# Kernel optimization log

Measured on AMD Instinct MI355X. Metric: run time of the kernel, lower is better.

Reference implementation:

```python
import jax, jax.numpy as jnp
import numpy as np
from functools import reduce

N_QUBITS = 6
DIM = 2 ** N_QUBITS  # 64

# PauliZ expectation signs per wire: zsign[j, q] = +1 if bit q of basis state j is 0 else -1
# PennyLane convention: wire 0 is the most-significant bit.
_ZSIGN = jnp.asarray(1.0 - 2.0 * ((np.arange(DIM)[:, None] >> (N_QUBITS - 1 - np.arange(N_QUBITS))[None, :]) & 1), dtype=jnp.float32)  # [64, 6]

def _cnot_perm(c, t):
    # permutation p with new_state[j] = old_state[p[j]] for CNOT(control=c, target=t)
    idx = np.arange(DIM)
    cbit = (idx >> (N_QUBITS - 1 - c)) & 1
    return idx ^ (cbit << (N_QUBITS - 1 - t))

def _ring_perm(r):
    # compose the ring of CNOTs: CNOT(w, (w+r)%n) for w = 0..n-1 applied in order
    total = np.arange(DIM)
    for w in range(N_QUBITS):
        total = total[_cnot_perm(w, (w + r) % N_QUBITS)]
    return total

_RING = {r: jnp.asarray(_ring_perm(r)) for r in (1, 2)}

def _rot(phi, theta, omega):
    # PennyLane Rot(phi, theta, omega) = RZ(omega) @ RY(theta) @ RZ(phi)
    c = jnp.cos(theta / 2.0)
    s = jnp.sin(theta / 2.0)
    em = jnp.exp(-0.5j * (phi + omega))
    ep = jnp.exp(0.5j * (phi - omega))
    return jnp.stack([jnp.stack([em * c, -ep * s]),
                      jnp.stack([jnp.conj(ep) * s, jnp.conj(em) * c])])

def _strongly_entangling(psi, theta):
    # theta: [L, N_QUBITS, 3]; psi: [B, 64] complex
    L = theta.shape[0]
    for l in range(L):
        mats = [_rot(theta[l, w, 0], theta[l, w, 1], theta[l, w, 2]) for w in range(N_QUBITS)]
        U = reduce(jnp.kron, mats)  # [64, 64]; wire 0 = most significant, matches kron order
        psi = psi @ U.T
        r = l % (N_QUBITS - 1) + 1  # PennyLane default ranges
        psi = psi[:, _RING[r]]
    return psi

def setup_inputs() -> dict:
    key = jax.random.key(0)
    ks = jax.random.split(key, 12)
    B, D, H, NW = 131072, 64, 64, 5
    return {
        'x': jax.random.normal(ks[0], (B, D), dtype=jnp.float32),
        'W1': jax.random.normal(ks[1], (H, D), dtype=jnp.float32) * 0.1,
        'b1': jnp.zeros((H,), dtype=jnp.float32),
        'ln_g': jnp.ones((H,), dtype=jnp.float32),
        'ln_b': jnp.zeros((H,), dtype=jnp.float32),
        'W2': jax.random.normal(ks[2], (N_QUBITS, H), dtype=jnp.float32) * 0.1,
        'b2': jnp.zeros((N_QUBITS,), dtype=jnp.float32),
        'theta_shared': jax.random.normal(ks[3], (2, N_QUBITS, 3), dtype=jnp.float32) * 0.1,
        'theta_task': jax.random.normal(ks[4], (1, N_QUBITS, 3), dtype=jnp.float32) * 0.1,
        'Wc': jax.random.normal(ks[5], (NW, N_QUBITS), dtype=jnp.float32) * 0.1,
        'bc': jnp.zeros((NW,), dtype=jnp.float32),
    }

def reference(x, W1, b1, ln_g, ln_b, W2, b2, theta_shared, theta_task, Wc, bc):
    # --- encoder: Linear -> ReLU -> LayerNorm -> Linear -> Tanh ---
    h = jax.nn.relu(x @ W1.T + b1)
    mu = h.mean(-1, keepdims=True)
    var = ((h - mu) ** 2).mean(-1, keepdims=True)
    h = (h - mu) / jnp.sqrt(var + 1e-5) * ln_g + ln_b
    z = jnp.tanh(h @ W2.T + b2)  # [B, 6], in [-1, 1]
    # --- amplitude prep: RY(pi * z_q) on |0> per qubit -> product state ---
    half = (jnp.pi * z) / 2.0
    vec = jnp.stack([jnp.cos(half), jnp.sin(half)], axis=-1)  # [B, 6, 2]
    psi = vec[:, 0]
    for q in range(1, N_QUBITS):
        psi = (psi[:, :, None] * vec[:, q][:, None, :]).reshape(psi.shape[0], -1)
    psi = psi.astype(jnp.complex64)  # [B, 64]
    # --- VQC layers ---
    psi = _strongly_entangling(psi, theta_shared)
    psi = _strongly_entangling(psi, theta_task)
    # --- PauliZ expectation per wire ---
    probs = (psi * jnp.conj(psi)).real  # [B, 64]
    q_out = probs @ _ZSIGN  # [B, 6]
    # --- linear classifier ---
    return q_out @ Wc.T + bc
```

## Files before the change

### kernel.cpp

```cpp
#include <hip/hip_runtime.h>
#include <utility>

#define NQ 6
#define DIM 64

namespace {

constexpr int ring_entry(int r, int i) {
    int idx = i;
    for (int w = NQ - 1; w >= 0; --w) {
        int c = w;
        int t = (w + r) % NQ;
        int cbit = (idx >> (NQ - 1 - c)) & 1;
        idx ^= cbit << (NQ - 1 - t);
    }
    return idx;
}

constexpr int Mc(int L, int i) {
    if (L == 1) return ring_entry(1, i);
    if (L == 2) return ring_entry(1, ring_entry(2, i));
    if (L == 3) return ring_entry(1, ring_entry(2, ring_entry(1, i)));
    return i;
}

constexpr int Minv(int L, int p) {
    for (int i = 0; i < DIM; ++i) if (Mc(L, i) == p) return i;
    return -1;
}

}

__device__ __forceinline__ float swap1(float v) {
    return __int_as_float(__builtin_amdgcn_mov_dpp(__float_as_int(v), 0xB1, 0xF, 0xF, true));
}


template<int LY, int W, int d, int... Ls>
__device__ __forceinline__ void wire_inlane(float* sr, float* si,
        float A0r, float A0i, float B0r, float B0i,
        float A1r, float A1i, float B1r, float B1i,
        std::integer_sequence<int, Ls...>) {
    (([&] {
        if constexpr (Ls < (Ls ^ d)) {
            constexpr int la = Ls, lb = Ls ^ d;
            constexpr int ra = (Minv(LY, la) >> (5 - W)) & 1;
            constexpr int rb = (Minv(LY, lb) >> (5 - W)) & 1;
            const float cAar = ra ? A1r : A0r, cAai = ra ? A1i : A0i;
            const float cBar = ra ? B1r : B0r, cBai = ra ? B1i : B0i;
            const float cAbr = rb ? A1r : A0r, cAbi = rb ? A1i : A0i;
            const float cBbr = rb ? B1r : B0r, cBbi = rb ? B1i : B0i;
            const float mar = sr[la], mai = si[la];
            const float mbr = sr[lb], mbi = si[lb];
            sr[la] = cAar*mar - cAai*mai + cBar*mbr - cBai*mbi;
            si[la] = cAar*mai + cAai*mar + cBar*mbi + cBai*mbr;
            sr[lb] = cAbr*mbr - cAbi*mbi + cBbr*mar - cBbi*mai;
            si[lb] = cAbr*mbi + cAbi*mbr + cBbr*mai + cBbi*mar;
        }
    }()), ...);
}

template<int LY, int W, int... Ls>
__device__ __forceinline__ void wire_cross0(float* sr, float* si,
        float A0r, float A0i, float B0r, float B0i,
        float A1r, float A1i, float B1r, float B1i,
        std::integer_sequence<int, Ls...>) {
    (([&] {
        constexpr int r = (Minv(LY, Ls) >> (5 - W)) & 1;
        const float cAr = r ? A1r : A0r, cAi = r ? A1i : A0i;
        const float cBr = r ? B1r : B0r, cBi = r ? B1i : B0i;
        const float mr = sr[Ls], mi = si[Ls];
        const float tr = swap1(mr), ti = swap1(mi);
        sr[Ls] = cAr*mr - cAi*mi + cBr*tr - cBi*ti;
        si[Ls] = cAr*mi + cAi*mr + cBr*ti + cBi*tr;
    }()), ...);
}

template<int LY, int W, int d, int... Ls>
__device__ __forceinline__ void wire_crossd(float* sr, float* si,
        float A0r, float A0i, float B0r, float B0i,
        float A1r, float A1i, float B1r, float B1i,
        std::integer_sequence<int, Ls...>) {
    (([&] {
        if constexpr (Ls < (Ls ^ d)) {
            constexpr int la = Ls, lb = Ls ^ d;
            constexpr int ra = (Minv(LY, la) >> (5 - W)) & 1;
            constexpr int rb = (Minv(LY, lb) >> (5 - W)) & 1;
            const float cAar = ra ? A1r : A0r, cAai = ra ? A1i : A0i;
            const float cBar = ra ? B1r : B0r, cBai = ra ? B1i : B0i;
            const float cAbr = rb ? A1r : A0r, cAbi = rb ? A1i : A0i;
            const float cBbr = rb ? B1r : B0r, cBbi = rb ? B1i : B0i;
            const float mar = sr[la], mai = si[la];
            const float mbr = sr[lb], mbi = si[lb];
            const float tar = swap1(mbr), tai_ = swap1(mbi);
            const float tbr = swap1(mar), tbi_ = swap1(mai);
            sr[la] = cAar*mar - cAai*mai + cBar*tar - cBai*tai_;
            si[la] = cAar*mai + cAai*mar + cBar*tai_ + cBai*tar;
            sr[lb] = cAbr*mbr - cAbi*mbi + cBbr*tbr - cBbi*tbi_;
            si[lb] = cAbr*mbi + cAbi*mbr + cBbr*tbi_ + cBbi*tbr;
        }
    }()), ...);
}

template<int LY, int W>
__device__ __forceinline__ void wire_apply(float* sr, float* si,
        const float* __restrict__ g, bool par) {
    constexpr int D = Mc(LY, 1 << (5 - W));
    constexpr bool cross = (D >> 5) & 1;
    constexpr int d = D & 31;
    constexpr bool cpar = (Minv(LY, 32) >> (5 - W)) & 1;

    float A0r, A0i, B0r, B0i, A1r, A1i, B1r, B1i;
    if constexpr (cpar) {
        A0r = par ? g[6] : g[0];  A0i = par ? g[7] : g[1];
        B0r = par ? g[4] : g[2];  B0i = par ? g[5] : g[3];
        A1r = par ? g[0] : g[6];  A1i = par ? g[1] : g[7];
        B1r = par ? g[2] : g[4];  B1i = par ? g[3] : g[5];
    } else {
        A0r = g[0]; A0i = g[1]; B0r = g[2]; B0i = g[3];
        A1r = g[6]; A1i = g[7]; B1r = g[4]; B1i = g[5];
    }
    if constexpr (!cross) {
        wire_inlane<LY, W, d>(sr, si, A0r, A0i, B0r, B0i, A1r, A1i, B1r, B1i,
                              std::make_integer_sequence<int, 32>{});
    } else if constexpr (d == 0) {
        wire_cross0<LY, W>(sr, si, A0r, A0i, B0r, B0i, A1r, A1i, B1r, B1i,
                           std::make_integer_sequence<int, 32>{});
    } else {
        wire_crossd<LY, W, d>(sr, si, A0r, A0i, B0r, B0i, A1r, A1i, B1r, B1i,
                              std::make_integer_sequence<int, 32>{});
    }
}

template<int LY>
__device__ __forceinline__ void layer_apply(float* sr, float* si,
        const float* __restrict__ g, bool par) {
    wire_apply<LY, 0>(sr, si, g,      par);
    wire_apply<LY, 1>(sr, si, g + 8,  par);
    wire_apply<LY, 2>(sr, si, g + 16, par);
    wire_apply<LY, 3>(sr, si, g + 24, par);
    wire_apply<LY, 4>(sr, si, g + 32, par);
    wire_apply<LY, 5>(sr, si, g + 40, par);
}

template<int... Ls>
__device__ __forceinline__ void readout_impl(const float* sr, const float* si, float* q,
                                             std::integer_sequence<int, Ls...>) {
    (([&] {
        constexpr int iv = Minv(3, Ls);
        const float pb = sr[Ls]*sr[Ls] + si[Ls]*si[Ls];
        q[0] += ((iv >> 5) & 1) ? -pb : pb;
        q[1] += ((iv >> 4) & 1) ? -pb : pb;
        q[2] += ((iv >> 3) & 1) ? -pb : pb;
        q[3] += ((iv >> 2) & 1) ? -pb : pb;
        q[4] += ((iv >> 1) & 1) ? -pb : pb;
        q[5] += ( iv       & 1) ? -pb : pb;
    }()), ...);
}

__device__ __forceinline__ void compute_gates6(const float* __restrict__ th, float* g) {
#pragma unroll
    for (int w = 0; w < NQ; ++w) {
        const float phi = th[w*3+0], theta = th[w*3+1], omega = th[w*3+2];
        float s, c, sa, ca, sb, cb;
        __sincosf(0.5f * theta, &s, &c);
        __sincosf(0.5f * (phi + omega), &sa, &ca);
        __sincosf(0.5f * (phi - omega), &sb, &cb);
        g[w*8+0] =  ca * c;  g[w*8+1] = -sa * c;
        g[w*8+2] = -cb * s;  g[w*8+3] = -sb * s;
        g[w*8+4] =  cb * s;  g[w*8+5] = -sb * s;
        g[w*8+6] =  ca * c;  g[w*8+7] =  sa * c;
    }
}

__global__ void setup_kernel(const float* __restrict__ th_s, const float* __restrict__ th_t,
                             const float* __restrict__ ln_g, const float* __restrict__ ln_b,
                             const float* __restrict__ W2, const float* __restrict__ b2,
                             float* __restrict__ ws) {
    const int t = threadIdx.x;
    if (t < 18) {
        const int l = t / 6, w = t % 6;
        const float* th = (l < 2) ? (th_s + (l * 6 + w) * 3) : (th_t + w * 3);
        const float phi = th[0], theta = th[1], omega = th[2];
        float s, c, sa, ca, sb, cb;
        sincosf(0.5f * theta, &s, &c);
        sincosf(0.5f * (phi + omega), &sa, &ca);
        sincosf(0.5f * (phi - omega), &sb, &cb);
        float* g = ws + t * 8;
        g[0] =  ca * c;  g[1] = -sa * c;
        g[2] = -cb * s;  g[3] = -sb * s;
        g[4] =  cb * s;  g[5] = -sb * s;
        g[6] =  ca * c;  g[7] =  sa * c;
    }
    if (t < 384) {
        const int j = t / 6, m = t % 6;
        ws[144 + t] = ln_g[j] * W2[m * 64 + j];
    }
    if (t < 6) {
        float c1 = 0.f, c2 = 0.f;
        for (int j = 0; j < 64; ++j) {
            c1 += ln_g[j] * W2[t * 64 + j];
            c2 += ln_b[j] * W2[t * 64 + j];
        }
        ws[528 + t] = c1;
        ws[534 + t] = c2 + b2[t];
    }
}

template<bool USE_WS>
__global__ __launch_bounds__(256, 4)
void qmaml_kernel(
    const float* __restrict__ x,  const float* __restrict__ W1, const float* __restrict__ b1,
    const float* __restrict__ ln_g, const float* __restrict__ ln_b,
    const float* __restrict__ W2, const float* __restrict__ b2,
    const float* __restrict__ th_s, const float* __restrict__ th_t,
    const float* __restrict__ Wc, const float* __restrict__ bc,
    const float* __restrict__ ws, float* __restrict__ out, int nrows) {

    const int t   = blockIdx.x * 256 + threadIdx.x;
    const int row = t >> 1;
    const bool par = t & 1;
    if (row >= nrows) return;

    float4 xv[16];
    const float4* xp = (const float4*)(x + (long)row * 64);
#pragma unroll
    for (int k = 0; k < 16; ++k) xv[k] = xp[k];

    float A[6]  = {0.f, 0.f, 0.f, 0.f, 0.f, 0.f};
    float C1[6] = {0.f, 0.f, 0.f, 0.f, 0.f, 0.f};
    float C2[6] = {0.f, 0.f, 0.f, 0.f, 0.f, 0.f};
    float s = 0.f, s2 = 0.f;

    for (int j = 0; j < 64; ++j) {
        const float4* wr = (const float4*)(W1 + j * 64);
        float acc = b1[j];
#pragma unroll
        for (int k = 0; k < 16; ++k) {
            const float4 w4 = wr[k];
            acc = fmaf(w4.x, xv[k].x, acc);
            acc = fmaf(w4.y, xv[k].y, acc);
            acc = fmaf(w4.z, xv[k].z, acc);
            acc = fmaf(w4.w, xv[k].w, acc);
        }
        acc = fmaxf(acc, 0.f);
        s += acc; s2 += acc * acc;
        if constexpr (USE_WS) {
            const float* Gt = ws + 144 + j * 6;
#pragma unroll
            for (int m = 0; m < 6; ++m) A[m] = fmaf(acc, Gt[m], A[m]);
        } else {
            const float gj = ln_g[j], bj = ln_b[j];
#pragma unroll
            for (int m = 0; m < 6; ++m) {
                const float w2 = W2[m * 64 + j];
                const float gw = gj * w2;
                A[m]  = fmaf(acc, gw, A[m]);
                C1[m] += gw;
                C2[m] = fmaf(bj, w2, C2[m]);
            }
        }
    }

    const float mu  = s  * (1.f / 64.f);
    const float var = s2 * (1.f / 64.f) - mu * mu;
    const float inv = rsqrtf(var + 1e-5f);

    float vc[6], vsn[6];
#pragma unroll
    for (int m = 0; m < 6; ++m) {
        float c1v, c2v;
        if constexpr (USE_WS) { c1v = ws[528 + m]; c2v = ws[534 + m]; }
        else                  { c1v = C1[m];       c2v = C2[m] + b2[m]; }
        const float zp = inv * (A[m] - mu * c1v) + c2v;
        const float e  = __expf(2.f * zp);
        const float z  = 1.f - 2.f / (e + 1.f);
        const float half = 1.57079632679f * z;
        vsn[m] = __sinf(half);
        vc[m]  = __cosf(half);
    }

    float gf[48];
    const float* g0;
    if constexpr (USE_WS) g0 = ws;
    else { compute_gates6(th_s, gf); g0 = gf; }

    float gar[6], gai[6], gbr[6], gbi[6];
#pragma unroll
    for (int w = 0; w < 6; ++w) {
        const float c = vc[w], sv = vsn[w];
        gar[w] = g0[w*8+0]*c + g0[w*8+2]*sv;
        gai[w] = g0[w*8+1]*c + g0[w*8+3]*sv;
        gbr[w] = g0[w*8+4]*c + g0[w*8+6]*sv;
        gbi[w] = g0[w*8+5]*c + g0[w*8+7]*sv;
    }

    float c1r_[2], c1i_[2];
    {
        const float c0r = par ? gbr[0] : gar[0];
        const float c0i = par ? gbi[0] : gai[0];
#pragma unroll
        for (int k = 0; k < 2; ++k) {
            const float yr = k ? gbr[1] : gar[1], yi = k ? gbi[1] : gai[1];
            c1r_[k] = c0r * yr - c0i * yi;
            c1i_[k] = c0r * yi + c0i * yr;
        }
    }
    float c2r_[4], c2i_[4];
#pragma unroll
    for (int k = 0; k < 4; ++k) {
        const int h = k >> 1, b = k & 1;
        const float yr = b ? gbr[2] : gar[2], yi = b ? gbi[2] : gai[2];
        c2r_[k] = c1r_[h] * yr - c1i_[h] * yi;
        c2i_[k] = c1r_[h] * yi + c1i_[h] * yr;
    }
    float c3r[8], c3i[8];
#pragma unroll
    for (int k = 0; k < 8; ++k) {
        const int h = k >> 1, b = k & 1;
        const float yr = b ? gbr[3] : gar[3], yi = b ? gbi[3] : gai[3];
        c3r[k] = c2r_[h] * yr - c2i_[h] * yi;
        c3i[k] = c2r_[h] * yi + c2i_[h] * yr;
    }
    float c4r[16], c4i[16];
#pragma unroll
    for (int k = 0; k < 16; ++k) {
        const int h = k >> 1, b = k & 1;
        const float yr = b ? gbr[4] : gar[4], yi = b ? gbi[4] : gai[4];
        c4r[k] = c3r[h] * yr - c3i[h] * yi;
        c4i[k] = c3r[h] * yi + c3i[h] * yr;
    }
    float sr[32], si[32];
#pragma unroll
    for (int k = 0; k < 32; ++k) {
        const int h = k >> 1, b = k & 1;
        const float yr = b ? gbr[5] : gar[5], yi = b ? gbi[5] : gai[5];
        sr[k] = c4r[h] * yr - c4i[h] * yi;
        si[k] = c4r[h] * yi + c4i[h] * yr;
    }

    if constexpr (USE_WS) {
        layer_apply<1>(sr, si, ws + 48, par);
        layer_apply<2>(sr, si, ws + 96, par);
    } else {
        compute_gates6(th_s + 18, gf);
        layer_apply<1>(sr, si, gf, par);
        compute_gates6(th_t, gf);
        layer_apply<2>(sr, si, gf, par);
    }

    float q[6] = {0.f, 0.f, 0.f, 0.f, 0.f, 0.f};
    readout_impl(sr, si, q, std::make_integer_sequence<int, 32>{});

    const float pm = par ? -1.f : 1.f;
    constexpr int invC = Minv(3, 32);
#pragma unroll
    for (int w = 0; w < 6; ++w) {
        float tq = q[w];
        if ((invC >> (5 - w)) & 1) tq *= pm;
        q[w] = tq + swap1(tq);
    }

    float o[5];
#pragma unroll
    for (int n = 0; n < 5; ++n) {
        float v = bc[n];
#pragma unroll
        for (int w = 0; w < 6; ++w) v = fmaf(q[w], Wc[n * 6 + w], v);
        o[n] = v;
    }
    float* orow = out + (long)row * 5;
    if (!par) { orow[0] = o[0]; orow[1] = o[1]; orow[2] = o[2]; }
    else      { orow[3] = o[3]; orow[4] = o[4]; }
}

extern "C" void kernel_launch(void* const* d_in, const int* in_sizes, int n_in,
                              void* d_out, int out_size, void* d_ws, size_t ws_size,
                              hipStream_t stream) {
    const float* x   = (const float*)d_in[0];
    const float* W1  = (const float*)d_in[1];
    const float* b1  = (const float*)d_in[2];
    const float* lng = (const float*)d_in[3];
    const float* lnb = (const float*)d_in[4];
    const float* W2  = (const float*)d_in[5];
    const float* b2  = (const float*)d_in[6];
    const float* ths = (const float*)d_in[7];
    const float* tht = (const float*)d_in[8];
    const float* Wc  = (const float*)d_in[9];
    const float* bc  = (const float*)d_in[10];
    float* out = (float*)d_out;
    float* ws  = (float*)d_ws;

    const int nrows = in_sizes[0] / 64;
    const int nthreads = nrows * 2;
    const int grid = (nthreads + 255) / 256;

    if (ws_size >= 540 * sizeof(float)) {
        setup_kernel<<<1, 384, 0, stream>>>(ths, tht, lng, lnb, W2, b2, ws);
        qmaml_kernel<true><<<grid, 256, 0, stream>>>(x, W1, b1, lng, lnb, W2, b2,
                                                     ths, tht, Wc, bc, ws, out, nrows);
    } else {
        qmaml_kernel<false><<<grid, 256, 0, stream>>>(x, W1, b1, lng, lnb, W2, b2,
                                                      ths, tht, Wc, bc, nullptr, out, nrows);
    }
}
```

Measured before the change: 155.9 us.

## Compute first linear layer with fp16 MFMA via LDS staging

Replaces the per-thread scalar FP32 x@W1^T dot products with fp16 32x32x16 MFMA instructions. Four waves per 512-thread block compute the ReLU hidden activations for 256 rows and stage them in shared memory. All threads then read those activations back for LayerNorm and the quantum-circuit simulation. The setup kernel pre-packs W1 into fp16 in MFMA operand layout. This trades FP32 precision on the encoder for matrix-core throughput, and adds a block barrier plus about 70KB of LDS per block, which limits occupancy.

```diff
diff --git a/kernel.cpp b/kernel.cpp
--- a/kernel.cpp
+++ b/kernel.cpp
@@ -31,8 +31,19 @@
 
 }
 
+typedef _Float16 h2_t  __attribute__((ext_vector_type(2)));
+typedef _Float16 f16x8 __attribute__((ext_vector_type(8)));
+typedef float    f32x16 __attribute__((ext_vector_type(16)));
+
 __device__ __forceinline__ float swap1(float v) {
     return __int_as_float(__builtin_amdgcn_mov_dpp(__float_as_int(v), 0xB1, 0xF, 0xF, true));
+}
+
+__device__ __forceinline__ f32x16 zero16() {
+    f32x16 v;
+#pragma unroll
+    for (int i = 0; i < 16; ++i) v[i] = 0.f;
+    return v;
 }
 
 
@@ -109,7 +120,6 @@
     constexpr bool cross = (D >> 5) & 1;
     constexpr int d = D & 31;
     constexpr bool cpar = (Minv(LY, 32) >> (5 - W)) & 1;
-
     float A0r, A0i, B0r, B0i, A1r, A1i, B1r, B1i;
     if constexpr (cpar) {
         A0r = par ? g[6] : g[0];  A0i = par ? g[7] : g[1];
@@ -173,10 +183,12 @@
     }
 }
 
-__global__ void setup_kernel(const float* __restrict__ th_s, const float* __restrict__ th_t,
-                             const float* __restrict__ ln_g, const float* __restrict__ ln_b,
-                             const float* __restrict__ W2, const float* __restrict__ b2,
-                             float* __restrict__ ws) {
+#define WS_NEED 3072
+
+__global__ void setup_hyb(const float* __restrict__ th_s, const float* __restrict__ th_t,
+                          const float* __restrict__ ln_g, const float* __restrict__ ln_b,
+                          const float* __restrict__ W1,  const float* __restrict__ W2,
+                          const float* __restrict__ b2,  float* __restrict__ ws) {
     const int t = threadIdx.x;
     if (t < 18) {
         const int l = t / 6, w = t % 6;
@@ -192,9 +204,9 @@
         g[4] =  cb * s;  g[5] = -sb * s;
         g[6] =  ca * c;  g[7] =  sa * c;
     }
-    if (t < 384) {
-        const int j = t / 6, m = t % 6;
-        ws[144 + t] = ln_g[j] * W2[m * 64 + j];
+    for (int s = t; s < 384; s += 256) {
+        const int j = s / 6, m = s % 6;
+        ws[144 + s] = ln_g[j] * W2[m * 64 + j];
     }
     if (t < 6) {
         float c1 = 0.f, c2 = 0.f;
@@ -205,17 +217,197 @@
         ws[528 + t] = c1;
         ws[534 + t] = c2 + b2[t];
     }
-}
-
-template<bool USE_WS>
+    for (int s = t; s < 512; s += 256) {
+        const int ks = s >> 7, nt = (s >> 6) & 1, ln = s & 63;
+        const int n = nt * 32 + (ln & 31);
+        union { _Float16 h[8]; float4 f; } u;
+        for (int j = 0; j < 8; ++j) {
+            const int k = ks * 16 + (ln >> 5) * 8 + j;
+            u.h[j] = (_Float16)W1[n * 64 + k];
+        }
+        ((float4*)(ws + 1024))[s] = u.f;
+    }
+}
+
+__global__ __launch_bounds__(512, 4)
+void qmaml_hybrid(const float* __restrict__ x, const float* __restrict__ b1,
+                  const float* __restrict__ Wc, const float* __restrict__ bc,
+                  const float* __restrict__ ws, float* __restrict__ out, int nrows) {
+    __shared__ __align__(16) float Hld[256 * 68];
+    const int tid  = threadIdx.x;
+    const int wv   = tid >> 6;
+    const int lane = tid & 63;
+    const int lm = lane & 31, lh = lane >> 5;
+    const long rowbase = (long)blockIdx.x * 256;
+
+    if (wv < 4) {
+        const float4* __restrict__ w1f = (const float4*)(ws + 1024);
+        const float bA = b1[lm], bB = b1[32 + lm];
+        float* Hw = Hld + (wv * 64) * 68;
+#pragma unroll
+        for (int t = 0; t < 2; ++t) {
+            long arow = rowbase + wv * 64 + t * 32 + lm;
+            if (arow >= nrows) arow = nrows - 1;
+            const float* xr = x + arow * 64 + lh * 8;
+            f16x8 a[4];
+#pragma unroll
+            for (int ks = 0; ks < 4; ++ks) {
+                const float4 q0 = *(const float4*)(xr + ks * 16);
+                const float4 q1 = *(const float4*)(xr + ks * 16 + 4);
+                a[ks][0] = (_Float16)q0.x; a[ks][1] = (_Float16)q0.y;
+                a[ks][2] = (_Float16)q0.z; a[ks][3] = (_Float16)q0.w;
+                a[ks][4] = (_Float16)q1.x; a[ks][5] = (_Float16)q1.y;
+                a[ks][6] = (_Float16)q1.z; a[ks][7] = (_Float16)q1.w;
+            }
+            f32x16 ac0 = zero16(), ac1 = zero16();
+#pragma unroll
+            for (int ks = 0; ks < 4; ++ks) {
+                union { float4 f; f16x8 h; } b0, b1v;
+                b0.f  = w1f[(ks * 2 + 0) * 64 + lane];
+                b1v.f = w1f[(ks * 2 + 1) * 64 + lane];
+                ac0 = __builtin_amdgcn_mfma_f32_32x32x16_f16(a[ks], b0.h,  ac0, 0, 0, 0);
+                ac1 = __builtin_amdgcn_mfma_f32_32x32x16_f16(a[ks], b1v.h, ac1, 0, 0, 0);
+            }
+#pragma unroll
+            for (int r = 0; r < 16; ++r) {
+                const int rl = t * 32 + (r & 3) + 8 * (r >> 2) + 4 * lh;
+                Hw[rl * 68 + lm]      = fmaxf(ac0[r] + bA, 0.f);
+                Hw[rl * 68 + 32 + lm] = fmaxf(ac1[r] + bB, 0.f);
+            }
+        }
+    }
+    __syncthreads();
+
+    const int row = tid >> 1;
+    const bool par = tid & 1;
+
+    float s = 0.f, s2 = 0.f;
+    float A[6] = {0.f, 0.f, 0.f, 0.f, 0.f, 0.f};
+    const float* __restrict__ Gt = ws + 144;
+    const float* hrow = Hld + row * 68;
+    for (int j4 = 0; j4 < 64; j4 += 4) {
+        const float4 hv = *(const float4*)(hrow + j4);
+        const float h0 = hv.x, h1 = hv.y, h2 = hv.z, h3 = hv.w;
+        s  += h0 + h1 + h2 + h3;
+        s2 += h0*h0 + h1*h1 + h2*h2 + h3*h3;
+#pragma unroll
+        for (int m = 0; m < 6; ++m) {
+            A[m] = fmaf(h0, Gt[(j4+0)*6+m], A[m]);
+            A[m] = fmaf(h1, Gt[(j4+1)*6+m], A[m]);
+            A[m] = fmaf(h2, Gt[(j4+2)*6+m], A[m]);
+            A[m] = fmaf(h3, Gt[(j4+3)*6+m], A[m]);
+        }
+    }
+
+    const float mu  = s  * (1.f / 64.f);
+    const float var = s2 * (1.f / 64.f) - mu * mu;
+    const float inv = rsqrtf(var + 1e-5f);
+
+    float vc[6], vsn[6];
+#pragma unroll
+    for (int m = 0; m < 6; ++m) {
+        const float zp = inv * (A[m] - mu * ws[528 + m]) + ws[534 + m];
+        const float e  = __expf(2.f * zp);
+        const float z  = 1.f - 2.f / (e + 1.f);
+        const float half = 1.57079632679f * z;
+        vsn[m] = __sinf(half);
+        vc[m]  = __cosf(half);
+    }
+
+    const float* __restrict__ g0 = ws;
+    float gar[6], gai[6], gbr[6], gbi[6];
+#pragma unroll
+    for (int w = 0; w < 6; ++w) {
+        const float c = vc[w], sv = vsn[w];
+        gar[w] = g0[w*8+0]*c + g0[w*8+2]*sv;
+        gai[w] = g0[w*8+1]*c + g0[w*8+3]*sv;
+        gbr[w] = g0[w*8+4]*c + g0[w*8+6]*sv;
+        gbi[w] = g0[w*8+5]*c + g0[w*8+7]*sv;
+    }
+
+    float c1r_[2], c1i_[2];
+    {
+        const float c0r = par ? gbr[0] : gar[0];
+        const float c0i = par ? gbi[0] : gai[0];
+#pragma unroll
+        for (int k = 0; k < 2; ++k) {
+            const float yr = k ? gbr[1] : gar[1], yi = k ? gbi[1] : gai[1];
+            c1r_[k] = c0r * yr - c0i * yi;
+            c1i_[k] = c0r * yi + c0i * yr;
+        }
+    }
+    float c2r_[4], c2i_[4];
+#pragma unroll
+    for (int k = 0; k < 4; ++k) {
+        const int h = k >> 1, b = k & 1;
+        const float yr = b ? gbr[2] : gar[2], yi = b ? gbi[2] : gai[2];
+        c2r_[k] = c1r_[h] * yr - c1i_[h] * yi;
+        c2i_[k] = c1r_[h] * yi + c1i_[h] * yr;
+    }
+    float c3r[8], c3i[8];
+#pragma unroll
+    for (int k = 0; k < 8; ++k) {
+        const int h = k >> 1, b = k & 1;
+        const float yr = b ? gbr[3] : gar[3], yi = b ? gbi[3] : gai[3];
+        c3r[k] = c2r_[h] * yr - c2i_[h] * yi;
+        c3i[k] = c2r_[h] * yi + c2i_[h] * yr;
+    }
+    float c4r[16], c4i[16];
+#pragma unroll
+    for (int k = 0; k < 16; ++k) {
+        const int h = k >> 1, b = k & 1;
+        const float yr = b ? gbr[4] : gar[4], yi = b ? gbi[4] : gai[4];
+        c4r[k] = c3r[h] * yr - c3i[h] * yi;
+        c4i[k] = c3r[h] * yi + c3i[h] * yr;
+    }
+    float sr[32], si[32];
+#pragma unroll
+    for (int k = 0; k < 32; ++k) {
+        const int h = k >> 1, b = k & 1;
+        const float yr = b ? gbr[5] : gar[5], yi = b ? gbi[5] : gai[5];
+        sr[k] = c4r[h] * yr - c4i[h] * yi;
+        si[k] = c4r[h] * yi + c4i[h] * yr;
+    }
+
+    layer_apply<1>(sr, si, ws + 48, par);
+    layer_apply<2>(sr, si, ws + 96, par);
+
+    float q[6] = {0.f, 0.f, 0.f, 0.f, 0.f, 0.f};
+    readout_impl(sr, si, q, std::make_integer_sequence<int, 32>{});
+
+    const float pm = par ? -1.f : 1.f;
+    constexpr int invC = Minv(3, 32);
+#pragma unroll
+    for (int w = 0; w < 6; ++w) {
+        float tq = q[w];
+        if ((invC >> (5 - w)) & 1) tq *= pm;
+        q[w] = tq + swap1(tq);
+    }
+
+    float o[5];
+#pragma unroll
+    for (int n = 0; n < 5; ++n) {
+        float v = bc[n];
+#pragma unroll
+        for (int w = 0; w < 6; ++w) v = fmaf(q[w], Wc[n * 6 + w], v);
+        o[n] = v;
+    }
+    const long orow = rowbase + row;
+    if (orow < nrows) {
+        float* op = out + orow * 5;
+        if (!par) { op[0] = o[0]; op[1] = o[1]; op[2] = o[2]; }
+        else      { op[3] = o[3]; op[4] = o[4]; }
+    }
+}
+
 __global__ __launch_bounds__(256, 4)
-void qmaml_kernel(
+void qmaml_fallback(
     const float* __restrict__ x,  const float* __restrict__ W1, const float* __restrict__ b1,
     const float* __restrict__ ln_g, const float* __restrict__ ln_b,
     const float* __restrict__ W2, const float* __restrict__ b2,
     const float* __restrict__ th_s, const float* __restrict__ th_t,
     const float* __restrict__ Wc, const float* __restrict__ bc,
-    const float* __restrict__ ws, float* __restrict__ out, int nrows) {
+    float* __restrict__ out, int nrows) {
 
     const int t   = blockIdx.x * 256 + threadIdx.x;
     const int row = t >> 1;
@@ -245,20 +437,14 @@
         }
         acc = fmaxf(acc, 0.f);
         s += acc; s2 += acc * acc;
-        if constexpr (USE_WS) {
-            const float* Gt = ws + 144 + j * 6;
-#pragma unroll
-            for (int m = 0; m < 6; ++m) A[m] = fmaf(acc, Gt[m], A[m]);
-        } else {
-            const float gj = ln_g[j], bj = ln_b[j];
-#pragma unroll
-            for (int m = 0; m < 6; ++m) {
-                const float w2 = W2[m * 64 + j];
-                const float gw = gj * w2;
-                A[m]  = fmaf(acc, gw, A[m]);
-                C1[m] += gw;
-                C2[m] = fmaf(bj, w2, C2[m]);
-            }
+        const float gj = ln_g[j], bj = ln_b[j];
+#pragma unroll
+        for (int m = 0; m < 6; ++m) {
+            const float w2 = W2[m * 64 + j];
+            const float gw = gj * w2;
+            A[m]  = fmaf(acc, gw, A[m]);
+            C1[m] += gw;
+            C2[m] = fmaf(bj, w2, C2[m]);
         }
     }
 
@@ -269,10 +455,7 @@
     float vc[6], vsn[6];
 #pragma unroll
     for (int m = 0; m < 6; ++m) {
-        float c1v, c2v;
-        if constexpr (USE_WS) { c1v = ws[528 + m]; c2v = ws[534 + m]; }
-        else                  { c1v = C1[m];       c2v = C2[m] + b2[m]; }
-        const float zp = inv * (A[m] - mu * c1v) + c2v;
+        const float zp = inv * (A[m] - mu * C1[m]) + C2[m] + b2[m];
         const float e  = __expf(2.f * zp);
         const float z  = 1.f - 2.f / (e + 1.f);
         const float half = 1.57079632679f * z;
@@ -281,18 +464,15 @@
     }
 
     float gf[48];
-    const float* g0;
-    if constexpr (USE_WS) g0 = ws;
-    else { compute_gates6(th_s, gf); g0 = gf; }
-
+    compute_gates6(th_s, gf);
     float gar[6], gai[6], gbr[6], gbi[6];
 #pragma unroll
     for (int w = 0; w < 6; ++w) {
         const float c = vc[w], sv = vsn[w];
-        gar[w] = g0[w*8+0]*c + g0[w*8+2]*sv;
-        gai[w] = g0[w*8+1]*c + g0[w*8+3]*sv;
-        gbr[w] = g0[w*8+4]*c + g0[w*8+6]*sv;
-        gbi[w] = g0[w*8+5]*c + g0[w*8+7]*sv;
+        gar[w] = gf[w*8+0]*c + gf[w*8+2]*sv;
+        gai[w] = gf[w*8+1]*c + gf[w*8+3]*sv;
+        gbr[w] = gf[w*8+4]*c + gf[w*8+6]*sv;
+        gbi[w] = gf[w*8+5]*c + gf[w*8+7]*sv;
     }
 
     float c1r_[2], c1i_[2];
@@ -339,15 +519,10 @@
         si[k] = c4r[h] * yi + c4i[h] * yr;
     }
 
-    if constexpr (USE_WS) {
-        layer_apply<1>(sr, si, ws + 48, par);
-        layer_apply<2>(sr, si, ws + 96, par);
-    } else {
-        compute_gates6(th_s + 18, gf);
-        layer_apply<1>(sr, si, gf, par);
-        compute_gates6(th_t, gf);
-        layer_apply<2>(sr, si, gf, par);
-    }
+    compute_gates6(th_s + 18, gf);
+    layer_apply<1>(sr, si, gf, par);
+    compute_gates6(th_t, gf);
+    layer_apply<2>(sr, si, gf, par);
 
     float q[6] = {0.f, 0.f, 0.f, 0.f, 0.f, 0.f};
     readout_impl(sr, si, q, std::make_integer_sequence<int, 32>{});
@@ -392,15 +567,14 @@
     float* ws  = (float*)d_ws;
 
     const int nrows = in_sizes[0] / 64;
-    const int nthreads = nrows * 2;
-    const int grid = (nthreads + 255) / 256;
-
-    if (ws_size >= 540 * sizeof(float)) {
-        setup_kernel<<<1, 384, 0, stream>>>(ths, tht, lng, lnb, W2, b2, ws);
-        qmaml_kernel<true><<<grid, 256, 0, stream>>>(x, W1, b1, lng, lnb, W2, b2,
-                                                     ths, tht, Wc, bc, ws, out, nrows);
+
+    if (ws_size >= WS_NEED * sizeof(float)) {
+        setup_hyb<<<1, 256, 0, stream>>>(ths, tht, lng, lnb, W1, W2, b2, ws);
+        const int blocks = (nrows + 255) / 256;
+        qmaml_hybrid<<<blocks, 512, 0, stream>>>(x, b1, Wc, bc, ws, out, nrows);
     } else {
-        qmaml_kernel<false><<<grid, 256, 0, stream>>>(x, W1, b1, lng, lnb, W2, b2,
-                                                      ths, tht, Wc, bc, nullptr, out, nrows);
-    }
-}
+        const int grid = (nrows * 2 + 255) / 256;
+        qmaml_fallback<<<grid, 256, 0, stream>>>(x, W1, b1, lng, lnb, W2, b2,
+                                                 ths, tht, Wc, bc, out, nrows);
+    }
+}
```

Result: slower. 299.0 us (+91.8%).
